# Optimization experiments

Hardware: AMD Instinct MI355X
Metric: run time of the kernel (lower is better)

## Reference

```python
import jax, jax.numpy as jnp
import numpy as np

N = 8192
C_IN = 512
C_INTER = 128  # in_channels // unit_nums = 512 // 4


def setup_inputs() -> dict:
    key = jax.random.key(0)
    ks = jax.random.split(key, 6)
    x = jax.random.normal(ks[0], (N, C_IN), dtype=jnp.float32)
    # Linear weights init: normal(0, 0.01); biases zero. Stored as [in, out].
    Wg = 0.01 * jax.random.normal(ks[1], (C_IN, C_INTER), dtype=jnp.float32)
    Wt = 0.01 * jax.random.normal(ks[2], (C_IN, C_INTER), dtype=jnp.float32)
    Wp = 0.01 * jax.random.normal(ks[3], (C_IN, C_INTER), dtype=jnp.float32)
    bg = jnp.zeros((C_INTER,), dtype=jnp.float32)
    bt = jnp.zeros((C_INTER,), dtype=jnp.float32)
    bp = jnp.zeros((C_INTER,), dtype=jnp.float32)
    # 1x1 conv weight (1, 2*C_INTER, 1, 1) flattened: first half hits theta, second half phi
    wcat = 0.01 * jax.random.normal(ks[4], (2 * C_INTER,), dtype=jnp.float32)
    return {"x": x, "Wg": Wg, "bg": bg, "Wt": Wt, "bt": bt, "Wp": Wp, "bp": bp, "wcat": wcat}


def reference(x, Wg, bg, Wt, bt, Wp, bp, wcat):
    n = x.shape[0]
    g_x = x @ Wg + bg          # [N, C_inter]
    theta = x @ Wt + bt        # [N, C_inter]
    phi = x @ Wp + bp          # [N, C_inter]
    c = theta.shape[1]
    # 1x1 conv over cat([theta_i, phi_j]) == w1.theta_i + w2.phi_j (outer sum), then ReLU
    a = theta @ wcat[:c]       # [N]
    b = phi @ wcat[c:]         # [N]
    f = jax.nn.relu(a[:, None] + b[None, :])  # [N, N]
    z = (f / n) @ g_x          # [N, C_inter]
    return z
```

## Files before the change

kernel.cpp:

```cpp
#include <hip/hip_runtime.h>

#define C_IN   512
#define C_INT  128
#define NBUCK  8192
#define SEG    32
#define NSEG   256

typedef short short8 __attribute__((ext_vector_type(8)));
typedef float floatx4 __attribute__((ext_vector_type(4)));


__device__ __forceinline__ int bucket_of(float v, float bmin, float inv_w) {
    float fk = (v - bmin) * inv_w;
    fk = fminf(fmaxf(fk, 0.f), (float)(NBUCK - 1));
    return (int)fk;
}

__device__ __forceinline__ short bf16rnd(float v) {
    unsigned u = __float_as_uint(v);
    return (short)((u + 0x7fffu + ((u >> 16) & 1u)) >> 16);
}


__global__ __launch_bounds__(256) void prep_kernel(
        const float* __restrict__ Wt, const float* __restrict__ Wp,
        const float* __restrict__ Wg, const float* __restrict__ wcat,
        const float* __restrict__ bt, const float* __restrict__ bp,
        float* __restrict__ ut, float* __restrict__ up, float* __restrict__ scal,
        unsigned short* __restrict__ WgT) {
    int t = threadIdx.x, bk = blockIdx.x;
    if (bk < 16) {
        const float* W  = (bk < 8) ? Wt : Wp;
        const float* wv = wcat + ((bk < 8) ? 0 : C_INT);
        float* dst      = (bk < 8) ? ut : up;
        int k = (bk & 7) * 64 + (t >> 2);
        int q = t & 3;
        const float4* row = (const float4*)(W + (size_t)k * C_INT);
        const float4* cv4 = (const float4*)wv;
        float s = 0.f;
        #pragma unroll
        for (int i = 0; i < 8; ++i) {
            float4 a = row[q * 8 + i];
            float4 c = cv4[q * 8 + i];
            s += a.x * c.x + a.y * c.y + a.z * c.z + a.w * c.w;
        }
        s += __shfl_xor(s, 1);
        s += __shfl_xor(s, 2);
        if (q == 0) dst[k] = s;
    } else if (bk == 16) {
        float s1p = (t < C_INT) ? bt[t] * wcat[t] : 0.f;
        float s2p = (t < C_INT) ? bp[t] * wcat[C_INT + t] : 0.f;
        for (int off = 32; off; off >>= 1) {
            s1p += __shfl_down(s1p, off);
            s2p += __shfl_down(s2p, off);
        }
        __shared__ float red[8];
        int w = t >> 6, lane = t & 63;
        if (lane == 0) { red[w] = s1p; red[4 + w] = s2p; }
        __syncthreads();
        if (t == 0) {
            scal[0] = red[0] + red[1] + red[2] + red[3];
            scal[1] = red[4] + red[5] + red[6] + red[7];
        }
    } else {
        __shared__ float tile[64][132];
        int kb = (bk - 17) * 64;
        #pragma unroll
        for (int it = 0; it < 8; ++it) {
            int idx = it * 256 + t;
            int r = idx >> 5, c4 = idx & 31;
            *(float4*)&tile[r][c4 * 4] =
                ((const float4*)(Wg + (size_t)(kb + r) * C_INT))[c4];
        }
        __syncthreads();
        int n = t & 127, kc = (t >> 7) * 32;
        unsigned pk[16];
        #pragma unroll
        for (int i = 0; i < 16; ++i) {
            unsigned lo = (unsigned short)bf16rnd(tile[kc + 2 * i][n]);
            unsigned hi = (unsigned short)bf16rnd(tile[kc + 2 * i + 1][n]);
            pk[i] = lo | (hi << 16);
        }
        uint4* dst = (uint4*)(WgT + (size_t)n * C_IN + kb + kc);
        #pragma unroll
        for (int i2 = 0; i2 < 4; ++i2) dst[i2] = *(uint4*)&pk[i2 * 4];
    }
}


#define RSTR 66

__global__ __launch_bounds__(256) void gemm_mfma(
        const float* __restrict__ x, const unsigned short* __restrict__ WgT,
        const float* __restrict__ bg,
        const float* __restrict__ ut, const float* __restrict__ up,
        const float* __restrict__ scal,
        _Float16* __restrict__ g, float* __restrict__ a, float* __restrict__ b) {
    __shared__ float red[3][20][RSTR];
    int tid = threadIdx.x;
    int lane = tid & 63, wv = tid >> 6;
    int bx = blockIdx.x;
    int i0 = (bx >> 1) * 16;
    int cg = bx & 1;
    int m = lane & 15, q = lane >> 4;
    floatx4 accg[4] = {};
    floatx4 accab = {};
    const float* xrow = x + (size_t)(i0 + m) * C_IN + q * 8;
    const float* absrc = (m == 0) ? ut : up;
    #pragma unroll
    for (int ks = 0; ks < 4; ++ks) {
        int k0 = (wv * 4 + ks) * 32;
        float4 f0 = *(const float4*)(xrow + k0);
        float4 f1 = *(const float4*)(xrow + k0 + 4);
        short8 af;
        af[0] = bf16rnd(f0.x); af[1] = bf16rnd(f0.y);
        af[2] = bf16rnd(f0.z); af[3] = bf16rnd(f0.w);
        af[4] = bf16rnd(f1.x); af[5] = bf16rnd(f1.y);
        af[6] = bf16rnd(f1.z); af[7] = bf16rnd(f1.w);
        if (cg == 0) {
            short8 abf = {};
            if (m < 2) {
                float4 u0 = *(const float4*)(absrc + k0 + q * 8);
                float4 u1 = *(const float4*)(absrc + k0 + q * 8 + 4);
                abf[0] = bf16rnd(u0.x); abf[1] = bf16rnd(u0.y);
                abf[2] = bf16rnd(u0.z); abf[3] = bf16rnd(u0.w);
                abf[4] = bf16rnd(u1.x); abf[5] = bf16rnd(u1.y);
                abf[6] = bf16rnd(u1.z); abf[7] = bf16rnd(u1.w);
            }
            accab = __builtin_amdgcn_mfma_f32_16x16x32_bf16(af, abf, accab, 0, 0, 0);
        }
        #pragma unroll
        for (int f = 0; f < 4; ++f) {
            short8 bfr = *(const short8*)(WgT + (size_t)(cg * 64 + f * 16 + m) * C_IN + k0 + q * 8);
            accg[f] = __builtin_amdgcn_mfma_f32_16x16x32_bf16(af, bfr, accg[f], 0, 0, 0);
        }
    }
    if (wv) {
        #pragma unroll
        for (int f = 0; f < 4; ++f)
            #pragma unroll
            for (int r = 0; r < 4; ++r)
                red[wv - 1][f * 4 + r][lane] = accg[f][r];
        #pragma unroll
        for (int r = 0; r < 4; ++r)
            red[wv - 1][16 + r][lane] = accab[r];
    }
    __syncthreads();
    if (wv == 0) {
        #pragma unroll
        for (int w = 0; w < 3; ++w) {
            #pragma unroll
            for (int f = 0; f < 4; ++f)
                #pragma unroll
                for (int r = 0; r < 4; ++r)
                    accg[f][r] += red[w][f * 4 + r][lane];
            #pragma unroll
            for (int r = 0; r < 4; ++r)
                accab[r] += red[w][16 + r][lane];
        }
        #pragma unroll
        for (int f = 0; f < 4; ++f) {
            int col = cg * 64 + f * 16 + m;
            float bgv = bg[col];
            #pragma unroll
            for (int r = 0; r < 4; ++r) {
                int row = i0 + q * 4 + r;
                g[(size_t)row * C_INT + col] = (_Float16)(accg[f][r] + bgv);
            }
        }
        if (cg == 0 && m < 2) {
            float off = m ? scal[1] : scal[0];
            float* dst = m ? b : a;
            #pragma unroll
            for (int r = 0; r < 4; ++r) dst[i0 + q * 4 + r] = accab[r] + off;
        }
    }
}


__global__ __launch_bounds__(1024) void sort_kernel(
        const float* __restrict__ b, float* __restrict__ scal,
        unsigned* __restrict__ offs_g, unsigned short* __restrict__ perm_g,
        float* __restrict__ bsort_g) {
    __shared__ unsigned oh[NBUCK / 2];
    __shared__ unsigned cur[NBUCK / 2];
    __shared__ unsigned short ls[8192];
    __shared__ unsigned wtu[16];
    __shared__ float smn[16], smx[16], sbp[2];
    int t = threadIdx.x, lane = t & 63, wv = t >> 6;
    #pragma unroll
    for (int r = 0; r < 4; ++r) { oh[t + r * 1024] = 0u; cur[t + r * 1024] = 0u; }
    float bv[8];
    float mn = 1e30f, mx = -1e30f;
    #pragma unroll
    for (int r = 0; r < 8; ++r) {
        bv[r] = b[t + r * 1024];
        mn = fminf(mn, bv[r]); mx = fmaxf(mx, bv[r]);
    }
    for (int off = 32; off; off >>= 1) {
        mn = fminf(mn, __shfl_down(mn, off));
        mx = fmaxf(mx, __shfl_down(mx, off));
    }
    if (lane == 0) { smn[wv] = mn; smx[wv] = mx; }
    __syncthreads();
    if (t == 0) {
        float gmn = smn[0], gmx = smx[0];
        #pragma unroll
        for (int i = 1; i < 16; ++i) {
            gmn = fminf(gmn, smn[i]); gmx = fmaxf(gmx, smx[i]);
        }
        float range = gmx - gmn;
        float iw = (range > 1e-30f) ? (float)NBUCK / range : 0.f;
        sbp[0] = gmn; sbp[1] = iw;
        scal[4] = gmn; scal[5] = iw;
    }
    __syncthreads();
    float bmin = sbp[0], inv_w = sbp[1];
    int kb[8];
    #pragma unroll
    for (int r = 0; r < 8; ++r) {
        kb[r] = bucket_of(bv[r], bmin, inv_w);
        atomicAdd(&oh[kb[r] >> 1], (kb[r] & 1) ? 0x10000u : 1u);
    }
    __syncthreads();
    unsigned h[8], p = 0;
    #pragma unroll
    for (int w = 0; w < 4; ++w) {
        unsigned word = oh[t * 4 + w];
        p += word & 0xffffu;  h[w * 2]     = p;
        p += word >> 16;      h[w * 2 + 1] = p;
    }
    unsigned v = p;
    #pragma unroll
    for (int d = 1; d < 64; d <<= 1) {
        unsigned u = __shfl_up(v, d);
        if (lane >= d) v += u;
    }
    if (lane == 63) wtu[wv] = v;
    __syncthreads();
    if (t < 16) {
        unsigned w = wtu[t];
        #pragma unroll
        for (int d = 1; d < 16; d <<= 1) {
            unsigned u = __shfl_up(w, d);
            if (t >= d) w += u;
        }
        wtu[t] = w;
    }
    __syncthreads();
    unsigned base = (v - p) + (wv ? wtu[wv - 1] : 0u);
    #pragma unroll
    for (int w = 0; w < 4; ++w) {
        unsigned lo = base + h[w * 2], hi = base + h[w * 2 + 1];
        oh[t * 4 + w] = lo | (hi << 16);
        offs_g[t * 8 + w * 2 + 1] = lo;
        offs_g[t * 8 + w * 2 + 2] = hi;
    }
    if (t == 0) offs_g[0] = 0u;
    __syncthreads();
    #pragma unroll
    for (int r = 0; r < 8; ++r) {
        int j = t + r * 1024;
        int k = kb[r];
        unsigned st = 0u;
        if (k > 0) {
            unsigned word = oh[(k - 1) >> 1];
            st = ((k - 1) & 1) ? (word >> 16) : (word & 0xffffu);
        }
        unsigned old = atomicAdd(&cur[k >> 1], (k & 1) ? 0x10000u : 1u);
        unsigned pos = (k & 1) ? (old >> 16) : (old & 0xffffu);
        ls[st + pos] = (unsigned short)j;
    }
    __syncthreads();
    #pragma unroll
    for (int r = 0; r < 8; ++r) {
        int e = t + r * 1024;
        int j = ls[e];
        perm_g[e] = (unsigned short)j;
        bsort_g[e] = b[j];
    }
}


__global__ __launch_bounds__(128) void segsum_kernel(
        const _Float16* __restrict__ g, const unsigned short* __restrict__ perm,
        const float* __restrict__ bsort,
        float* __restrict__ seg1, float* __restrict__ seg2) {
    __shared__ int pj[SEG];
    __shared__ float pb[SEG];
    int s = blockIdx.x, t = threadIdx.x;
    if (t < SEG) { pj[t] = perm[s * SEG + t]; pb[t] = bsort[s * SEG + t]; }
    __syncthreads();
    float a1 = 0.f, a2 = 0.f;
    #pragma unroll
    for (int e = 0; e < SEG; ++e) {
        float gv = (float)g[(size_t)pj[e] * C_INT + t];
        a1 += gv; a2 += pb[e] * gv;
    }
    seg1[s * C_INT + t] = a1;
    seg2[s * C_INT + t] = a2;
}


__global__ __launch_bounds__(128) void expand_kernel(
        const _Float16* __restrict__ g, const unsigned short* __restrict__ perm,
        const float* __restrict__ bsort,
        const float* __restrict__ seg1, const float* __restrict__ seg2,
        float* __restrict__ Pr1, float* __restrict__ Pr2) {
    __shared__ int pj[SEG];
    __shared__ float pb[SEG];
    int s = blockIdx.x, t = threadIdx.x;
    if (t < SEG) { pj[t] = perm[s * SEG + t]; pb[t] = bsort[s * SEG + t]; }
    __syncthreads();
    float r1 = 0.f, r2 = 0.f;
    for (int s2 = s + 1; s2 < NSEG; ++s2) {
        r1 += seg1[s2 * C_INT + t];
        r2 += seg2[s2 * C_INT + t];
    }
    #pragma unroll
    for (int e = SEG - 1; e >= 0; --e) {
        float gv = (float)g[(size_t)pj[e] * C_INT + t];
        r1 += gv; r2 += pb[e] * gv;
        size_t idx = (size_t)(s * SEG + e) * C_INT + t;
        Pr1[idx] = r1; Pr2[idx] = r2;
    }
    if (s == NSEG - 1) {
        Pr1[(size_t)8192 * C_INT + t] = 0.f;
        Pr2[(size_t)8192 * C_INT + t] = 0.f;
    }
}


__global__ __launch_bounds__(128) void out_kernel(
        const float* __restrict__ a, const float* __restrict__ scal,
        const _Float16* __restrict__ g,
        const unsigned* __restrict__ offs, const unsigned short* __restrict__ perm,
        const float* __restrict__ bsort,
        const float* __restrict__ Pr1, const float* __restrict__ Pr2,
        float* __restrict__ out, float inv_n) {
    __shared__ int pj[128];
    __shared__ float pb[128];
    int i = blockIdx.x, c = threadIdx.x;
    float ai = a[i], thr = -ai;
    float bmin = scal[4], inv_w = scal[5];
    int ki = bucket_of(thr, bmin, inv_w);
    unsigned e0 = offs[ki], e1 = offs[ki + 1];
    size_t base = (size_t)e1 * C_INT + c;
    float acc = ai * Pr1[base] + Pr2[base];
    for (unsigned be = e0; be < e1; be += 128) {
        unsigned cnt = min(128u, e1 - be);
        if ((unsigned)c < cnt) { pj[c] = perm[be + c]; pb[c] = bsort[be + c]; }
        __syncthreads();
        for (unsigned r = 0; r < cnt; ++r) {
            float bj = pb[r];
            if (bj > thr)
                acc += (ai + bj) * (float)g[(size_t)pj[r] * C_INT + c];
        }
        __syncthreads();
    }
    out[(size_t)i * C_INT + c] = acc * inv_n;
}


extern "C" void kernel_launch(void* const* d_in, const int* in_sizes, int n_in,
                              void* d_out, int out_size, void* d_ws, size_t ws_size,
                              hipStream_t stream) {
    const float* x    = (const float*)d_in[0];
    const float* Wg   = (const float*)d_in[1];
    const float* bg   = (const float*)d_in[2];
    const float* Wt   = (const float*)d_in[3];
    const float* bt   = (const float*)d_in[4];
    const float* Wp   = (const float*)d_in[5];
    const float* bp   = (const float*)d_in[6];
    const float* wcat = (const float*)d_in[7];
    float* out = (float*)d_out;
    int n = in_sizes[0] / C_IN;

    char* w = (char*)d_ws;
    size_t off = 0;
    auto alloc = [&](size_t bytes) -> void* {
        void* p = w + off;
        off += (bytes + 255) & ~(size_t)255;
        return p;
    };
    float*          ut    = (float*)alloc(C_IN * 4);
    float*          up    = (float*)alloc(C_IN * 4);
    float*          scal  = (float*)alloc(32);
    float*          a     = (float*)alloc((size_t)n * 4);
    float*          b     = (float*)alloc((size_t)n * 4);
    unsigned*       offs  = (unsigned*)alloc((size_t)(NBUCK + 1) * 4);
    unsigned short* perm  = (unsigned short*)alloc((size_t)n * 2);
    float*          bsort = (float*)alloc((size_t)n * 4);
    _Float16*       g     = (_Float16*)alloc((size_t)n * C_INT * 2);
    unsigned short* WgT   = (unsigned short*)alloc((size_t)C_INT * C_IN * 2);
    float*          seg1  = (float*)alloc((size_t)NSEG * C_INT * 4);
    float*          seg2  = (float*)alloc((size_t)NSEG * C_INT * 4);
    float*          Pr1   = (float*)alloc((size_t)(n + 1) * C_INT * 4);
    float*          Pr2   = (float*)alloc((size_t)(n + 1) * C_INT * 4);

    prep_kernel<<<25, 256, 0, stream>>>(Wt, Wp, Wg, wcat, bt, bp, ut, up, scal, WgT);
    gemm_mfma<<<n / 8, 256, 0, stream>>>(x, WgT, bg, ut, up, scal, g, a, b);
    sort_kernel<<<1, 1024, 0, stream>>>(b, scal, offs, perm, bsort);
    segsum_kernel<<<NSEG, 128, 0, stream>>>(g, perm, bsort, seg1, seg2);
    expand_kernel<<<NSEG, 128, 0, stream>>>(g, perm, bsort, seg1, seg2, Pr1, Pr2);
    out_kernel<<<n, 128, 0, stream>>>(a, scal, g, offs, perm, bsort, Pr1, Pr2,
                                      out, 1.0f / (float)n);
}
```

Baseline: 143.6 us.

## Replace single-block sort and segment kernels with one cooperative grid kernel

The single-block 1024-thread counting sort, the segment-sum kernel and the expand kernel are merged into one cooperative kernel across 256 blocks. Global min/max now comes from atomics on order-preserving float keys, and the histogram, prefix offsets and scatter use global atomics separated by grid syncs. The gathered g values are kept in registers between the segment-sum and expand phases so they are not reloaded. The aim is to remove the serialized one-block sort and two launches, at the cost of several grid-wide barriers, global atomic contention, and a scatter order within buckets that is no longer deterministic.

Result: slower. 268.2 us (+86.8%).

```diff
diff --git a/kernel.cpp b/kernel.cpp
--- a/kernel.cpp
+++ b/kernel.cpp
@@ -1,4 +1,5 @@
 #include <hip/hip_runtime.h>
+#include <hip/hip_cooperative_groups.h>
 
 #define C_IN   512
 #define C_INT  128
@@ -6,6 +7,8 @@
 #define SEG    32
 #define NSEG   256
 
+namespace cg = cooperative_groups;
+
 typedef short short8 __attribute__((ext_vector_type(8)));
 typedef float floatx4 __attribute__((ext_vector_type(4)));
 
@@ -19,6 +22,15 @@
 __device__ __forceinline__ short bf16rnd(float v) {
     unsigned u = __float_as_uint(v);
     return (short)((u + 0x7fffu + ((u >> 16) & 1u)) >> 16);
+}
+
+__device__ __forceinline__ unsigned fkey(float f) {
+    unsigned u = __float_as_uint(f);
+    return (u & 0x80000000u) ? ~u : (u | 0x80000000u);
+}
+__device__ __forceinline__ float fdecode(unsigned k) {
+    unsigned u = (k & 0x80000000u) ? (k ^ 0x80000000u) : ~k;
+    return __uint_as_float(u);
 }
 
 
@@ -27,7 +39,8 @@
         const float* __restrict__ Wg, const float* __restrict__ wcat,
         const float* __restrict__ bt, const float* __restrict__ bp,
         float* __restrict__ ut, float* __restrict__ up, float* __restrict__ scal,
-        unsigned short* __restrict__ WgT) {
+        unsigned short* __restrict__ WgT,
+        unsigned* __restrict__ hist, unsigned* __restrict__ blocksum) {
     int t = threadIdx.x, bk = blockIdx.x;
     if (bk < 16) {
         const float* W  = (bk < 8) ? Wt : Wp;
@@ -61,8 +74,10 @@
         if (t == 0) {
             scal[0] = red[0] + red[1] + red[2] + red[3];
             scal[1] = red[4] + red[5] + red[6] + red[7];
-        }
-    } else {
+            ((unsigned*)scal)[6] = 0xFFFFFFFFu;
+            ((unsigned*)scal)[7] = 0u;
+        }
+    } else if (bk < 25) {
         __shared__ float tile[64][132];
         int kb = (bk - 17) * 64;
         #pragma unroll
@@ -84,6 +99,12 @@
         uint4* dst = (uint4*)(WgT + (size_t)n * C_IN + kb + kc);
         #pragma unroll
         for (int i2 = 0; i2 < 4; ++i2) dst[i2] = *(uint4*)&pk[i2 * 4];
+    } else {
+        uint4 z = {0u, 0u, 0u, 0u};
+        uint4* h4 = (uint4*)hist;
+        #pragma unroll
+        for (int i = 0; i < 8; ++i) h4[t + i * 256] = z;
+        if (t < 64) ((uint4*)blocksum)[t] = z;
     }
 }
 
@@ -101,7 +122,7 @@
     int lane = tid & 63, wv = tid >> 6;
     int bx = blockIdx.x;
     int i0 = (bx >> 1) * 16;
-    int cg = bx & 1;
+    int cg2 = bx & 1;
     int m = lane & 15, q = lane >> 4;
     floatx4 accg[4] = {};
     floatx4 accab = {};
@@ -117,7 +138,7 @@
         af[2] = bf16rnd(f0.z); af[3] = bf16rnd(f0.w);
         af[4] = bf16rnd(f1.x); af[5] = bf16rnd(f1.y);
         af[6] = bf16rnd(f1.z); af[7] = bf16rnd(f1.w);
-        if (cg == 0) {
+        if (cg2 == 0) {
             short8 abf = {};
             if (m < 2) {
                 float4 u0 = *(const float4*)(absrc + k0 + q * 8);
@@ -131,7 +152,7 @@
         }
         #pragma unroll
         for (int f = 0; f < 4; ++f) {
-            short8 bfr = *(const short8*)(WgT + (size_t)(cg * 64 + f * 16 + m) * C_IN + k0 + q * 8);
+            short8 bfr = *(const short8*)(WgT + (size_t)(cg2 * 64 + f * 16 + m) * C_IN + k0 + q * 8);
             accg[f] = __builtin_amdgcn_mfma_f32_16x16x32_bf16(af, bfr, accg[f], 0, 0, 0);
         }
     }
@@ -160,7 +181,7 @@
         }
         #pragma unroll
         for (int f = 0; f < 4; ++f) {
-            int col = cg * 64 + f * 16 + m;
+            int col = cg2 * 64 + f * 16 + m;
             float bgv = bg[col];
             #pragma unroll
             for (int r = 0; r < 4; ++r) {
@@ -168,7 +189,7 @@
                 g[(size_t)row * C_INT + col] = (_Float16)(accg[f][r] + bgv);
             }
         }
-        if (cg == 0 && m < 2) {
+        if (cg2 == 0 && m < 2) {
             float off = m ? scal[1] : scal[0];
             float* dst = m ? b : a;
             #pragma unroll
@@ -178,155 +199,110 @@
 }
 
 
-__global__ __launch_bounds__(1024) void sort_kernel(
+__global__ __launch_bounds__(128) void mid_kernel(
         const float* __restrict__ b, float* __restrict__ scal,
-        unsigned* __restrict__ offs_g, unsigned short* __restrict__ perm_g,
-        float* __restrict__ bsort_g) {
-    __shared__ unsigned oh[NBUCK / 2];
-    __shared__ unsigned cur[NBUCK / 2];
-    __shared__ unsigned short ls[8192];
-    __shared__ unsigned wtu[16];
-    __shared__ float smn[16], smx[16], sbp[2];
-    int t = threadIdx.x, lane = t & 63, wv = t >> 6;
-    #pragma unroll
-    for (int r = 0; r < 4; ++r) { oh[t + r * 1024] = 0u; cur[t + r * 1024] = 0u; }
-    float bv[8];
-    float mn = 1e30f, mx = -1e30f;
-    #pragma unroll
-    for (int r = 0; r < 8; ++r) {
-        bv[r] = b[t + r * 1024];
-        mn = fminf(mn, bv[r]); mx = fmaxf(mx, bv[r]);
-    }
-    for (int off = 32; off; off >>= 1) {
-        mn = fminf(mn, __shfl_down(mn, off));
-        mx = fmaxf(mx, __shfl_down(mx, off));
-    }
-    if (lane == 0) { smn[wv] = mn; smx[wv] = mx; }
-    __syncthreads();
-    if (t == 0) {
-        float gmn = smn[0], gmx = smx[0];
-        #pragma unroll
-        for (int i = 1; i < 16; ++i) {
-            gmn = fminf(gmn, smn[i]); gmx = fmaxf(gmx, smx[i]);
-        }
-        float range = gmx - gmn;
-        float iw = (range > 1e-30f) ? (float)NBUCK / range : 0.f;
-        sbp[0] = gmn; sbp[1] = iw;
-        scal[4] = gmn; scal[5] = iw;
-    }
-    __syncthreads();
-    float bmin = sbp[0], inv_w = sbp[1];
-    int kb[8];
-    #pragma unroll
-    for (int r = 0; r < 8; ++r) {
-        kb[r] = bucket_of(bv[r], bmin, inv_w);
-        atomicAdd(&oh[kb[r] >> 1], (kb[r] & 1) ? 0x10000u : 1u);
-    }
-    __syncthreads();
-    unsigned h[8], p = 0;
-    #pragma unroll
-    for (int w = 0; w < 4; ++w) {
-        unsigned word = oh[t * 4 + w];
-        p += word & 0xffffu;  h[w * 2]     = p;
-        p += word >> 16;      h[w * 2 + 1] = p;
-    }
-    unsigned v = p;
-    #pragma unroll
-    for (int d = 1; d < 64; d <<= 1) {
-        unsigned u = __shfl_up(v, d);
-        if (lane >= d) v += u;
-    }
-    if (lane == 63) wtu[wv] = v;
-    __syncthreads();
-    if (t < 16) {
-        unsigned w = wtu[t];
-        #pragma unroll
-        for (int d = 1; d < 16; d <<= 1) {
-            unsigned u = __shfl_up(w, d);
-            if (t >= d) w += u;
-        }
-        wtu[t] = w;
-    }
-    __syncthreads();
-    unsigned base = (v - p) + (wv ? wtu[wv - 1] : 0u);
-    #pragma unroll
-    for (int w = 0; w < 4; ++w) {
-        unsigned lo = base + h[w * 2], hi = base + h[w * 2 + 1];
-        oh[t * 4 + w] = lo | (hi << 16);
-        offs_g[t * 8 + w * 2 + 1] = lo;
-        offs_g[t * 8 + w * 2 + 2] = hi;
-    }
-    if (t == 0) offs_g[0] = 0u;
-    __syncthreads();
-    #pragma unroll
-    for (int r = 0; r < 8; ++r) {
-        int j = t + r * 1024;
-        int k = kb[r];
-        unsigned st = 0u;
-        if (k > 0) {
-            unsigned word = oh[(k - 1) >> 1];
-            st = ((k - 1) & 1) ? (word >> 16) : (word & 0xffffu);
-        }
-        unsigned old = atomicAdd(&cur[k >> 1], (k & 1) ? 0x10000u : 1u);
-        unsigned pos = (k & 1) ? (old >> 16) : (old & 0xffffu);
-        ls[st + pos] = (unsigned short)j;
-    }
-    __syncthreads();
-    #pragma unroll
-    for (int r = 0; r < 8; ++r) {
-        int e = t + r * 1024;
-        int j = ls[e];
-        perm_g[e] = (unsigned short)j;
-        bsort_g[e] = b[j];
-    }
-}
-
-
-__global__ __launch_bounds__(128) void segsum_kernel(
-        const _Float16* __restrict__ g, const unsigned short* __restrict__ perm,
-        const float* __restrict__ bsort,
-        float* __restrict__ seg1, float* __restrict__ seg2) {
+        unsigned* __restrict__ hist, unsigned* __restrict__ offs_g,
+        unsigned* __restrict__ blocksum,
+        unsigned short* __restrict__ perm_g, float* __restrict__ bsort_g,
+        const _Float16* __restrict__ g,
+        float* __restrict__ seg1, float* __restrict__ seg2,
+        float* __restrict__ Pr1, float* __restrict__ Pr2) {
+    cg::grid_group grid = cg::this_grid();
+    int s = blockIdx.x, t = threadIdx.x;
+
+    float bv = 0.f;
+    if (t < SEG) {
+        bv = b[s * SEG + t];
+        float mn = bv, mx = bv;
+        #pragma unroll
+        for (int d = 16; d; d >>= 1) {
+            mn = fminf(mn, __shfl_xor(mn, d));
+            mx = fmaxf(mx, __shfl_xor(mx, d));
+        }
+        if (t == 0) {
+            atomicMin(&((unsigned*)scal)[6], fkey(mn));
+            atomicMax(&((unsigned*)scal)[7], fkey(mx));
+        }
+    }
+    grid.sync();
+
+    float gmn = fdecode(((const unsigned*)scal)[6]);
+    float gmx = fdecode(((const unsigned*)scal)[7]);
+    float range = gmx - gmn;
+    float iw = (range > 1e-30f) ? (float)NBUCK / range : 0.f;
+    if (s == 0 && t == 0) { scal[4] = gmn; scal[5] = iw; }
+    int k = 0;
+    if (t < SEG) {
+        k = bucket_of(bv, gmn, iw);
+        atomicAdd(&hist[k], 1u);
+        atomicAdd(&blocksum[k >> 5], 1u);
+    }
+    grid.sync();
+
+    unsigned v = 0;
+    if (t < 32) {
+        v = hist[s * 32 + t];
+        #pragma unroll
+        for (int d = 1; d < 32; d <<= 1) {
+            unsigned u = __shfl_up(v, d);
+            if (t >= d) v += u;
+        }
+    }
+    unsigned base = 0;
+    if (t < 64) {
+        unsigned acc = 0;
+        #pragma unroll
+        for (int i = 0; i < 4; ++i) {
+            int idx = t + i * 64;
+            if (idx < s) acc += blocksum[idx];
+        }
+        #pragma unroll
+        for (int d = 32; d; d >>= 1) acc += __shfl_xor(acc, d);
+        base = acc;
+    }
+    if (t < 32) offs_g[s * 32 + t + 1] = base + v;
+    if (s == 0 && t == 0) offs_g[0] = 0u;
+    grid.sync();
+
+    if (t < SEG) {
+        unsigned st = offs_g[k];
+        unsigned pos = atomicSub(&hist[k], 1u) - 1u;
+        unsigned e = st + pos;
+        perm_g[e] = (unsigned short)(s * SEG + t);
+        bsort_g[e] = bv;
+    }
+    grid.sync();
+
     __shared__ int pj[SEG];
     __shared__ float pb[SEG];
-    int s = blockIdx.x, t = threadIdx.x;
-    if (t < SEG) { pj[t] = perm[s * SEG + t]; pb[t] = bsort[s * SEG + t]; }
+    if (t < SEG) { pj[t] = perm_g[s * SEG + t]; pb[t] = bsort_g[s * SEG + t]; }
     __syncthreads();
+    float gv[SEG];
     float a1 = 0.f, a2 = 0.f;
     #pragma unroll
     for (int e = 0; e < SEG; ++e) {
-        float gv = (float)g[(size_t)pj[e] * C_INT + t];
-        a1 += gv; a2 += pb[e] * gv;
+        gv[e] = (float)g[(size_t)pj[e] * C_INT + t];
+        a1 += gv[e]; a2 += pb[e] * gv[e];
     }
     seg1[s * C_INT + t] = a1;
     seg2[s * C_INT + t] = a2;
-}
-
-
-__global__ __launch_bounds__(128) void expand_kernel(
-        const _Float16* __restrict__ g, const unsigned short* __restrict__ perm,
-        const float* __restrict__ bsort,
-        const float* __restrict__ seg1, const float* __restrict__ seg2,
-        float* __restrict__ Pr1, float* __restrict__ Pr2) {
-    __shared__ int pj[SEG];
-    __shared__ float pb[SEG];
-    int s = blockIdx.x, t = threadIdx.x;
-    if (t < SEG) { pj[t] = perm[s * SEG + t]; pb[t] = bsort[s * SEG + t]; }
-    __syncthreads();
+    grid.sync();
+
     float r1 = 0.f, r2 = 0.f;
+    #pragma unroll 4
     for (int s2 = s + 1; s2 < NSEG; ++s2) {
         r1 += seg1[s2 * C_INT + t];
         r2 += seg2[s2 * C_INT + t];
     }
     #pragma unroll
     for (int e = SEG - 1; e >= 0; --e) {
-        float gv = (float)g[(size_t)pj[e] * C_INT + t];
-        r1 += gv; r2 += pb[e] * gv;
+        r1 += gv[e]; r2 += pb[e] * gv[e];
         size_t idx = (size_t)(s * SEG + e) * C_INT + t;
         Pr1[idx] = r1; Pr2[idx] = r2;
     }
     if (s == NSEG - 1) {
-        Pr1[(size_t)8192 * C_INT + t] = 0.f;
-        Pr2[(size_t)8192 * C_INT + t] = 0.f;
+        Pr1[(size_t)NBUCK * C_INT + t] = 0.f;
+        Pr2[(size_t)NBUCK * C_INT + t] = 0.f;
     }
 }
 
@@ -397,12 +373,31 @@
     float*          seg2  = (float*)alloc((size_t)NSEG * C_INT * 4);
     float*          Pr1   = (float*)alloc((size_t)(n + 1) * C_INT * 4);
     float*          Pr2   = (float*)alloc((size_t)(n + 1) * C_INT * 4);
-
-    prep_kernel<<<25, 256, 0, stream>>>(Wt, Wp, Wg, wcat, bt, bp, ut, up, scal, WgT);
+    unsigned*       hist  = (unsigned*)alloc((size_t)NBUCK * 4);
+    unsigned*       bsum  = (unsigned*)alloc((size_t)NSEG * 4);
+
+    prep_kernel<<<26, 256, 0, stream>>>(Wt, Wp, Wg, wcat, bt, bp, ut, up, scal,
+                                        WgT, hist, bsum);
     gemm_mfma<<<n / 8, 256, 0, stream>>>(x, WgT, bg, ut, up, scal, g, a, b);
-    sort_kernel<<<1, 1024, 0, stream>>>(b, scal, offs, perm, bsort);
-    segsum_kernel<<<NSEG, 128, 0, stream>>>(g, perm, bsort, seg1, seg2);
-    expand_kernel<<<NSEG, 128, 0, stream>>>(g, perm, bsort, seg1, seg2, Pr1, Pr2);
+
+    {
+        void* margs[12];
+        margs[0]  = (void*)&b;
+        margs[1]  = (void*)&scal;
+        margs[2]  = (void*)&hist;
+        margs[3]  = (void*)&offs;
+        margs[4]  = (void*)&bsum;
+        margs[5]  = (void*)&perm;
+        margs[6]  = (void*)&bsort;
+        margs[7]  = (void*)&g;
+        margs[8]  = (void*)&seg1;
+        margs[9]  = (void*)&seg2;
+        margs[10] = (void*)&Pr1;
+        margs[11] = (void*)&Pr2;
+        hipLaunchCooperativeKernel(mid_kernel, dim3(NSEG), dim3(128),
+                                   margs, 0, stream);
+    }
+
     out_kernel<<<n, 128, 0, stream>>>(a, scal, g, offs, perm, bsort, Pr1, Pr2,
                                       out, 1.0f / (float)n);
 }
```

## Split gemm across waves by output columns instead of K with LDS reduction

Applied to the files above, without the earlier changes.

The projection GEMM previously split K across four waves and reduced the partial sums through shared memory with a barrier, launching two blocks per 16-row tile. Now each block handles one 16-row tile and each wave computes a 32-column slice over the full K, so the shared-memory reduction and __syncthreads are gone. In exchange, each x row is loaded and converted to bf16 by all four waves (4x redundant x reads within a block), and the grid is halved.

After: 148.3 us. 3.3% more time.

```diff
diff --git a/kernel.cpp b/kernel.cpp
--- a/kernel.cpp
+++ b/kernel.cpp
@@ -88,28 +88,26 @@
 }
 
 
-#define RSTR 66
-
 __global__ __launch_bounds__(256) void gemm_mfma(
         const float* __restrict__ x, const unsigned short* __restrict__ WgT,
         const float* __restrict__ bg,
         const float* __restrict__ ut, const float* __restrict__ up,
         const float* __restrict__ scal,
         _Float16* __restrict__ g, float* __restrict__ a, float* __restrict__ b) {
-    __shared__ float red[3][20][RSTR];
     int tid = threadIdx.x;
     int lane = tid & 63, wv = tid >> 6;
-    int bx = blockIdx.x;
-    int i0 = (bx >> 1) * 16;
-    int cg = bx & 1;
+    int i0 = blockIdx.x * 16;
     int m = lane & 15, q = lane >> 4;
-    floatx4 accg[4] = {};
+    int wc = wv * 32;
+    floatx4 accg[2] = {};
     floatx4 accab = {};
     const float* xrow = x + (size_t)(i0 + m) * C_IN + q * 8;
     const float* absrc = (m == 0) ? ut : up;
-    #pragma unroll
-    for (int ks = 0; ks < 4; ++ks) {
-        int k0 = (wv * 4 + ks) * 32;
+    const unsigned short* b0p = WgT + (size_t)(wc + m) * C_IN + q * 8;
+    const unsigned short* b1p = WgT + (size_t)(wc + 16 + m) * C_IN + q * 8;
+    #pragma unroll 8
+    for (int ks = 0; ks < 16; ++ks) {
+        int k0 = ks * 32;
         float4 f0 = *(const float4*)(xrow + k0);
         float4 f1 = *(const float4*)(xrow + k0 + 4);
         short8 af;
@@ -117,7 +115,7 @@
         af[2] = bf16rnd(f0.z); af[3] = bf16rnd(f0.w);
         af[4] = bf16rnd(f1.x); af[5] = bf16rnd(f1.y);
         af[6] = bf16rnd(f1.z); af[7] = bf16rnd(f1.w);
-        if (cg == 0) {
+        if (wv == 0) {
             short8 abf = {};
             if (m < 2) {
                 float4 u0 = *(const float4*)(absrc + k0 + q * 8);
@@ -129,51 +127,26 @@
             }
             accab = __builtin_amdgcn_mfma_f32_16x16x32_bf16(af, abf, accab, 0, 0, 0);
         }
-        #pragma unroll
-        for (int f = 0; f < 4; ++f) {
-            short8 bfr = *(const short8*)(WgT + (size_t)(cg * 64 + f * 16 + m) * C_IN + k0 + q * 8);
-            accg[f] = __builtin_amdgcn_mfma_f32_16x16x32_bf16(af, bfr, accg[f], 0, 0, 0);
-        }
-    }
-    if (wv) {
-        #pragma unroll
-        for (int f = 0; f < 4; ++f)
-            #pragma unroll
-            for (int r = 0; r < 4; ++r)
-                red[wv - 1][f * 4 + r][lane] = accg[f][r];
-        #pragma unroll
-        for (int r = 0; r < 4; ++r)
-            red[wv - 1][16 + r][lane] = accab[r];
-    }
-    __syncthreads();
-    if (wv == 0) {
-        #pragma unroll
-        for (int w = 0; w < 3; ++w) {
-            #pragma unroll
-            for (int f = 0; f < 4; ++f)
-                #pragma unroll
-                for (int r = 0; r < 4; ++r)
-                    accg[f][r] += red[w][f * 4 + r][lane];
-            #pragma unroll
-            for (int r = 0; r < 4; ++r)
-                accab[r] += red[w][16 + r][lane];
-        }
-        #pragma unroll
-        for (int f = 0; f < 4; ++f) {
-            int col = cg * 64 + f * 16 + m;
-            float bgv = bg[col];
-            #pragma unroll
-            for (int r = 0; r < 4; ++r) {
-                int row = i0 + q * 4 + r;
-                g[(size_t)row * C_INT + col] = (_Float16)(accg[f][r] + bgv);
-            }
-        }
-        if (cg == 0 && m < 2) {
-            float off = m ? scal[1] : scal[0];
-            float* dst = m ? b : a;
-            #pragma unroll
-            for (int r = 0; r < 4; ++r) dst[i0 + q * 4 + r] = accab[r] + off;
-        }
+        short8 bf0 = *(const short8*)(b0p + k0);
+        short8 bf1 = *(const short8*)(b1p + k0);
+        accg[0] = __builtin_amdgcn_mfma_f32_16x16x32_bf16(af, bf0, accg[0], 0, 0, 0);
+        accg[1] = __builtin_amdgcn_mfma_f32_16x16x32_bf16(af, bf1, accg[1], 0, 0, 0);
+    }
+    #pragma unroll
+    for (int f = 0; f < 2; ++f) {
+        int col = wc + f * 16 + m;
+        float bgv = bg[col];
+        #pragma unroll
+        for (int r = 0; r < 4; ++r) {
+            int row = i0 + q * 4 + r;
+            g[(size_t)row * C_INT + col] = (_Float16)(accg[f][r] + bgv);
+        }
+    }
+    if (wv == 0 && m < 2) {
+        float off = m ? scal[1] : scal[0];
+        float* dst = m ? b : a;
+        #pragma unroll
+        for (int r = 0; r < 4; ++r) dst[i0 + q * 4 + r] = accab[r] + off;
     }
 }
 
@@ -399,7 +372,7 @@
     float*          Pr2   = (float*)alloc((size_t)(n + 1) * C_INT * 4);
 
     prep_kernel<<<25, 256, 0, stream>>>(Wt, Wp, Wg, wcat, bt, bp, ut, up, scal, WgT);
-    gemm_mfma<<<n / 8, 256, 0, stream>>>(x, WgT, bg, ut, up, scal, g, a, b);
+    gemm_mfma<<<n / 16, 256, 0, stream>>>(x, WgT, bg, ut, up, scal, g, a, b);
     sort_kernel<<<1, 1024, 0, stream>>>(b, scal, offs, perm, bsort);
     segsum_kernel<<<NSEG, 128, 0, stream>>>(g, perm, bsort, seg1, seg2);
     expand_kernel<<<NSEG, 128, 0, stream>>>(g, perm, bsort, seg1, seg2, Pr1, Pr2);
```

## Replace per-element prefix arrays with per-segment suffix sums and regrid GEMM

Applied to the files above, without the earlier changes.

Drops the kernel that materialized full per-element suffix sums of g and b·g (two large N×C arrays) and instead computes per-segment suffix sums in a single small kernel. The output kernel then finishes the partial segment by directly gathering the remaining rows of g, and drops the shared-memory staging and barriers. This removes megabytes of global writes and reads but adds up to a segment's worth of gathered rows per output row. The GEMM is also split four ways over output columns with more blocks to raise parallelism.

Result: faster. 140.4 us, median of 2 (-2.3%).

```diff
diff --git a/kernel.cpp b/kernel.cpp
--- a/kernel.cpp
+++ b/kernel.cpp
@@ -96,14 +96,14 @@
         const float* __restrict__ ut, const float* __restrict__ up,
         const float* __restrict__ scal,
         _Float16* __restrict__ g, float* __restrict__ a, float* __restrict__ b) {
-    __shared__ float red[3][20][RSTR];
+    __shared__ float red[3][12][RSTR];
     int tid = threadIdx.x;
     int lane = tid & 63, wv = tid >> 6;
     int bx = blockIdx.x;
-    int i0 = (bx >> 1) * 16;
-    int cg = bx & 1;
+    int cg2 = bx >> 9;
+    int i0 = (bx & 511) * 16;
     int m = lane & 15, q = lane >> 4;
-    floatx4 accg[4] = {};
+    floatx4 accg[2] = {};
     floatx4 accab = {};
     const float* xrow = x + (size_t)(i0 + m) * C_IN + q * 8;
     const float* absrc = (m == 0) ? ut : up;
@@ -117,7 +117,7 @@
         af[2] = bf16rnd(f0.z); af[3] = bf16rnd(f0.w);
         af[4] = bf16rnd(f1.x); af[5] = bf16rnd(f1.y);
         af[6] = bf16rnd(f1.z); af[7] = bf16rnd(f1.w);
-        if (cg == 0) {
+        if (cg2 == 0) {
             short8 abf = {};
             if (m < 2) {
                 float4 u0 = *(const float4*)(absrc + k0 + q * 8);
@@ -130,37 +130,37 @@
             accab = __builtin_amdgcn_mfma_f32_16x16x32_bf16(af, abf, accab, 0, 0, 0);
         }
         #pragma unroll
-        for (int f = 0; f < 4; ++f) {
-            short8 bfr = *(const short8*)(WgT + (size_t)(cg * 64 + f * 16 + m) * C_IN + k0 + q * 8);
+        for (int f = 0; f < 2; ++f) {
+            short8 bfr = *(const short8*)(WgT + (size_t)(cg2 * 32 + f * 16 + m) * C_IN + k0 + q * 8);
             accg[f] = __builtin_amdgcn_mfma_f32_16x16x32_bf16(af, bfr, accg[f], 0, 0, 0);
         }
     }
     if (wv) {
         #pragma unroll
-        for (int f = 0; f < 4; ++f)
+        for (int f = 0; f < 2; ++f)
             #pragma unroll
             for (int r = 0; r < 4; ++r)
                 red[wv - 1][f * 4 + r][lane] = accg[f][r];
         #pragma unroll
         for (int r = 0; r < 4; ++r)
-            red[wv - 1][16 + r][lane] = accab[r];
+            red[wv - 1][8 + r][lane] = accab[r];
     }
     __syncthreads();
     if (wv == 0) {
         #pragma unroll
         for (int w = 0; w < 3; ++w) {
             #pragma unroll
-            for (int f = 0; f < 4; ++f)
+            for (int f = 0; f < 2; ++f)
                 #pragma unroll
                 for (int r = 0; r < 4; ++r)
                     accg[f][r] += red[w][f * 4 + r][lane];
             #pragma unroll
             for (int r = 0; r < 4; ++r)
-                accab[r] += red[w][16 + r][lane];
-        }
-        #pragma unroll
-        for (int f = 0; f < 4; ++f) {
-            int col = cg * 64 + f * 16 + m;
+                accab[r] += red[w][8 + r][lane];
+        }
+        #pragma unroll
+        for (int f = 0; f < 2; ++f) {
+            int col = cg2 * 32 + f * 16 + m;
             float bgv = bg[col];
             #pragma unroll
             for (int r = 0; r < 4; ++r) {
@@ -168,7 +168,7 @@
                 g[(size_t)row * C_INT + col] = (_Float16)(accg[f][r] + bgv);
             }
         }
-        if (cg == 0 && m < 2) {
+        if (cg2 == 0 && m < 2) {
             float off = m ? scal[1] : scal[0];
             float* dst = m ? b : a;
             #pragma unroll
@@ -302,31 +302,33 @@
 }
 
 
-__global__ __launch_bounds__(128) void expand_kernel(
-        const _Float16* __restrict__ g, const unsigned short* __restrict__ perm,
-        const float* __restrict__ bsort,
+__global__ __launch_bounds__(1024) void sufseg_kernel(
         const float* __restrict__ seg1, const float* __restrict__ seg2,
-        float* __restrict__ Pr1, float* __restrict__ Pr2) {
-    __shared__ int pj[SEG];
-    __shared__ float pb[SEG];
-    int s = blockIdx.x, t = threadIdx.x;
-    if (t < SEG) { pj[t] = perm[s * SEG + t]; pb[t] = bsort[s * SEG + t]; }
+        float* __restrict__ Suf1, float* __restrict__ Suf2) {
+    __shared__ float ps1[8][128], ps2[8][128];
+    int t = threadIdx.x, u = t >> 7, c = t & 127;
+    float p1 = 0.f, p2 = 0.f;
+    #pragma unroll 8
+    for (int j = 0; j < 32; ++j) {
+        int s = u * 32 + j;
+        p1 += seg1[s * C_INT + c];
+        p2 += seg2[s * C_INT + c];
+    }
+    ps1[u][c] = p1; ps2[u][c] = p2;
     __syncthreads();
     float r1 = 0.f, r2 = 0.f;
-    for (int s2 = s + 1; s2 < NSEG; ++s2) {
-        r1 += seg1[s2 * C_INT + t];
-        r2 += seg2[s2 * C_INT + t];
-    }
-    #pragma unroll
-    for (int e = SEG - 1; e >= 0; --e) {
-        float gv = (float)g[(size_t)pj[e] * C_INT + t];
-        r1 += gv; r2 += pb[e] * gv;
-        size_t idx = (size_t)(s * SEG + e) * C_INT + t;
-        Pr1[idx] = r1; Pr2[idx] = r2;
-    }
-    if (s == NSEG - 1) {
-        Pr1[(size_t)8192 * C_INT + t] = 0.f;
-        Pr2[(size_t)8192 * C_INT + t] = 0.f;
+    #pragma unroll
+    for (int u2 = u + 1; u2 < 8; ++u2) { r1 += ps1[u2][c]; r2 += ps2[u2][c]; }
+    for (int j = 31; j >= 0; --j) {
+        int s = u * 32 + j;
+        r1 += seg1[s * C_INT + c];
+        r2 += seg2[s * C_INT + c];
+        Suf1[s * C_INT + c] = r1;
+        Suf2[s * C_INT + c] = r2;
+    }
+    if (t < 128) {
+        Suf1[256 * C_INT + t] = 0.f; Suf2[256 * C_INT + t] = 0.f;
+        Suf1[257 * C_INT + t] = 0.f; Suf2[257 * C_INT + t] = 0.f;
     }
 }
 
@@ -336,27 +338,28 @@
         const _Float16* __restrict__ g,
         const unsigned* __restrict__ offs, const unsigned short* __restrict__ perm,
         const float* __restrict__ bsort,
-        const float* __restrict__ Pr1, const float* __restrict__ Pr2,
+        const float* __restrict__ Suf1, const float* __restrict__ Suf2,
         float* __restrict__ out, float inv_n) {
-    __shared__ int pj[128];
-    __shared__ float pb[128];
     int i = blockIdx.x, c = threadIdx.x;
     float ai = a[i], thr = -ai;
     float bmin = scal[4], inv_w = scal[5];
     int ki = bucket_of(thr, bmin, inv_w);
     unsigned e0 = offs[ki], e1 = offs[ki + 1];
-    size_t base = (size_t)e1 * C_INT + c;
-    float acc = ai * Pr1[base] + Pr2[base];
-    for (unsigned be = e0; be < e1; be += 128) {
-        unsigned cnt = min(128u, e1 - be);
-        if ((unsigned)c < cnt) { pj[c] = perm[be + c]; pb[c] = bsort[be + c]; }
-        __syncthreads();
-        for (unsigned r = 0; r < cnt; ++r) {
-            float bj = pb[r];
-            if (bj > thr)
-                acc += (ai + bj) * (float)g[(size_t)pj[r] * C_INT + c];
-        }
-        __syncthreads();
+    unsigned s1 = e1 >> 5;
+    unsigned segend = min((s1 + 1u) * 32u, (unsigned)NBUCK);
+    size_t sb = (size_t)(s1 + 1u) * C_INT + c;
+    float acc = ai * Suf1[sb] + Suf2[sb];
+    for (unsigned e = e1; e < segend; ++e) {
+        float bj = bsort[e];
+        int j = perm[e];
+        acc += (ai + bj) * (float)g[(size_t)j * C_INT + c];
+    }
+    for (unsigned e = e0; e < e1; ++e) {
+        float bj = bsort[e];
+        if (bj > thr) {
+            int j = perm[e];
+            acc += (ai + bj) * (float)g[(size_t)j * C_INT + c];
+        }
     }
     out[(size_t)i * C_INT + c] = acc * inv_n;
 }
@@ -395,14 +398,14 @@
     unsigned short* WgT   = (unsigned short*)alloc((size_t)C_INT * C_IN * 2);
     float*          seg1  = (float*)alloc((size_t)NSEG * C_INT * 4);
     float*          seg2  = (float*)alloc((size_t)NSEG * C_INT * 4);
-    float*          Pr1   = (float*)alloc((size_t)(n + 1) * C_INT * 4);
-    float*          Pr2   = (float*)alloc((size_t)(n + 1) * C_INT * 4);
+    float*          Suf1  = (float*)alloc((size_t)258 * C_INT * 4);
+    float*          Suf2  = (float*)alloc((size_t)258 * C_INT * 4);
 
     prep_kernel<<<25, 256, 0, stream>>>(Wt, Wp, Wg, wcat, bt, bp, ut, up, scal, WgT);
-    gemm_mfma<<<n / 8, 256, 0, stream>>>(x, WgT, bg, ut, up, scal, g, a, b);
+    gemm_mfma<<<2048, 256, 0, stream>>>(x, WgT, bg, ut, up, scal, g, a, b);
     sort_kernel<<<1, 1024, 0, stream>>>(b, scal, offs, perm, bsort);
     segsum_kernel<<<NSEG, 128, 0, stream>>>(g, perm, bsort, seg1, seg2);
-    expand_kernel<<<NSEG, 128, 0, stream>>>(g, perm, bsort, seg1, seg2, Pr1, Pr2);
-    out_kernel<<<n, 128, 0, stream>>>(a, scal, g, offs, perm, bsort, Pr1, Pr2,
+    sufseg_kernel<<<1, 1024, 0, stream>>>(seg1, seg2, Suf1, Suf2);
+    out_kernel<<<n, 128, 0, stream>>>(a, scal, g, offs, perm, bsort, Suf1, Suf2,
                                       out, 1.0f / (float)n);
 }
```
